# Kernel tuning notes

Measured on AMD Instinct MI355X. Metric: run time of the kernel, lower is better.

The kernel has to match this reference:

```python
import jax, jax.numpy as jnp
import numpy as np

D_MODEL = 1024; D_STATE = 64; D_CONV = 4; EXPAND = 2; HEADDIM = 128; NGROUPS = 1; CHUNK = 256
D_INNER = EXPAND * D_MODEL            # 2048
NHEADS = D_INNER // HEADDIM           # 16
CONV_DIM = D_INNER + 2 * NGROUPS * D_STATE   # 2176
D_IN_PROJ = 2 * D_INNER + 2 * NGROUPS * D_STATE + NHEADS  # 4240
B = 4; G = 256; L = 2048
EPS = 1e-5


def setup_inputs() -> dict:
    key = jax.random.key(0)
    ks = jax.random.split(key, 12)
    def nrm(k, shape, s=0.02):
        return jax.random.normal(k, shape, jnp.float32) * s
    return dict(
        local_repr=jax.random.normal(ks[0], (B, L, D_MODEL), jnp.float32),
        global_repr=jax.random.normal(ks[1], (B, G, D_MODEL), jnp.float32),
        norm1_w=jnp.ones((D_MODEL,), jnp.float32), norm1_b=jnp.zeros((D_MODEL,), jnp.float32),
        norm2_w=jnp.ones((D_MODEL,), jnp.float32), norm2_b=jnp.zeros((D_MODEL,), jnp.float32),
        norm3_w=jnp.ones((D_MODEL,), jnp.float32), norm3_b=jnp.zeros((D_MODEL,), jnp.float32),
        in_proj_w=nrm(ks[2], (D_IN_PROJ, D_MODEL)),
        conv_w=nrm(ks[3], (CONV_DIM, D_CONV), 0.2),
        conv_b=jnp.zeros((CONV_DIM,), jnp.float32),
        dt_bias=jnp.log(jnp.expm1(jax.random.uniform(ks[4], (NHEADS,), jnp.float32, 1e-3, 0.1))),
        A_log=jnp.log(jax.random.uniform(ks[5], (NHEADS,), jnp.float32, 1.0, 16.0)),
        D_skip=jnp.ones((NHEADS,), jnp.float32),
        ssd_norm_w=jnp.ones((D_INNER,), jnp.float32),
        out_proj_w=nrm(ks[6], (D_MODEL, D_INNER)),
        ffn_w1=nrm(ks[7], (D_MODEL // 2, D_MODEL)),
        ffn_b1=jnp.zeros((D_MODEL // 2,), jnp.float32),
        ffn_w2=nrm(ks[8], (D_MODEL, D_MODEL // 2)),
        ffn_b2=jnp.zeros((D_MODEL,), jnp.float32),
    )


def _ln(x, w, b):
    mu = jnp.mean(x, axis=-1, keepdims=True)
    var = jnp.mean((x - mu) ** 2, axis=-1, keepdims=True)
    return (x - mu) * jax.lax.rsqrt(var + EPS) * w + b


def _segsum(a):
    # a: (..., T) -> (..., T, T) lower-triangular sums a[j+1..i]
    T = a.shape[-1]
    cs = jnp.cumsum(a, axis=-1)
    diff = cs[..., :, None] - cs[..., None, :]
    mask = jnp.tril(jnp.ones((T, T), bool))
    return jnp.where(mask, diff, -jnp.inf)


def _ssd(xdt, a_dt, Bh, Ch):
    # xdt: (b,t,h,p) = x*dt ; a_dt: (b,t,h) = dt*A ; Bh,Ch: (b,t,h,n)
    b, t, h, p = xdt.shape
    n = Bh.shape[-1]
    c = t // CHUNK
    X = xdt.reshape(b, c, CHUNK, h, p)
    Bc = Bh.reshape(b, c, CHUNK, h, n)
    Cc = Ch.reshape(b, c, CHUNK, h, n)
    Ac = a_dt.reshape(b, c, CHUNK, h).transpose(0, 3, 1, 2)  # (b,h,c,k)
    A_cum = jnp.cumsum(Ac, axis=-1)
    Lm = jnp.exp(_segsum(Ac))                                # (b,h,c,k,k)
    Y_diag = jnp.einsum('bckhn,bcshn,bhcks,bcshp->bckhp', Cc, Bc, Lm, X)
    decay_states = jnp.exp(A_cum[..., -1:] - A_cum)          # (b,h,c,k)
    states = jnp.einsum('bckhn,bhck,bckhp->bchpn', Bc, decay_states, X)
    A_last = jnp.pad(A_cum[..., -1], ((0, 0), (0, 0), (1, 0)))
    decay_chunk = jnp.exp(_segsum(A_last))                   # (b,h,c+1,c+1)
    states = jnp.concatenate([jnp.zeros_like(states[:, :1]), states], axis=1)
    new_states = jnp.einsum('bhzc,bchpn->bzhpn', decay_chunk, states)
    states_in = new_states[:, :-1]                           # (b,c,h,p,n)
    out_decay = jnp.exp(A_cum)                               # (b,h,c,k)
    Y_off = jnp.einsum('bckhn,bchpn,bhck->bckhp', Cc, states_in, out_decay)
    return (Y_diag + Y_off).reshape(b, t, h, p)


def _mamba2(x, in_proj_w, conv_w, conv_b, dt_bias, A_log, D_skip, ssd_norm_w, out_proj_w):
    b, t, _ = x.shape
    zxbcdt = x @ in_proj_w.T                                  # (b,t,D_IN_PROJ)
    z = zxbcdt[..., :D_INNER]
    xBC = zxbcdt[..., D_INNER:D_INNER + CONV_DIM]
    dt = jax.nn.softplus(zxbcdt[..., D_INNER + CONV_DIM:] + dt_bias)  # (b,t,h)
    # causal depthwise conv1d, kernel D_CONV
    xp = jnp.pad(xBC, ((0, 0), (D_CONV - 1, 0), (0, 0)))
    xBC = sum(xp[:, i:i + t, :] * conv_w[:, i] for i in range(D_CONV)) + conv_b
    xBC = jax.nn.silu(xBC)
    xs = xBC[..., :D_INNER].reshape(b, t, NHEADS, HEADDIM)
    Bm = xBC[..., D_INNER:D_INNER + NGROUPS * D_STATE].reshape(b, t, NGROUPS, D_STATE)
    Cm = xBC[..., D_INNER + NGROUPS * D_STATE:].reshape(b, t, NGROUPS, D_STATE)
    rep = NHEADS // NGROUPS
    Bh = jnp.repeat(Bm, rep, axis=2)
    Ch = jnp.repeat(Cm, rep, axis=2)
    A = -jnp.exp(A_log)                                       # (h,)
    Y = _ssd(xs * dt[..., None], dt * A, Bh, Ch)
    y = Y + D_skip[None, None, :, None] * xs
    y = y.reshape(b, t, D_INNER)
    # gated RMSNorm (norm_before_gate=False)
    y = y * jax.nn.silu(z)
    y = y * jax.lax.rsqrt(jnp.mean(y * y, axis=-1, keepdims=True) + EPS) * ssd_norm_w
    return y @ out_proj_w.T


def reference(local_repr, global_repr, norm1_w, norm1_b, norm2_w, norm2_b, norm3_w, norm3_b,
              in_proj_w, conv_w, conv_b, dt_bias, A_log, D_skip, ssd_norm_w, out_proj_w,
              ffn_w1, ffn_b1, ffn_w2, ffn_b2):
    local_n = _ln(local_repr, norm1_w, norm1_b)
    global_n = _ln(global_repr, norm2_w, norm2_b)
    x = jnp.concatenate([global_n, local_n], axis=1)          # (B, G+L, D)
    x = _mamba2(x, in_proj_w, conv_w, conv_b, dt_bias, A_log, D_skip, ssd_norm_w, out_proj_w)
    x = x[:, -local_n.shape[1]:, :] + local_n
    x = _ln(x, norm3_w, norm3_b)
    h = jax.nn.gelu(x @ ffn_w1.T + ffn_b1, approximate=False)
    return (h @ ffn_w2.T + ffn_b2) + x
```

## Files before the change

kernel.cpp:

```cpp
#include <hip/hip_runtime.h>
#include <math.h>

#define B_ 4
#define L_ 2048
#define G_ 256
#define T_ 2304
#define DM 1024
#define DINNER 2048
#define NH 16
#define HD 128
#define NSTATE 64
#define CONVD 2176
#define DPROJ 4240
#define NPROJ_PAD 4352
#define NCHUNK 9
#define CK 256
#define EPSV 1e-5f
#define CROWS 16

typedef unsigned short bf16t;
using bf16x8 = __attribute__((ext_vector_type(8))) short;
using f32x4  = __attribute__((ext_vector_type(4))) float;

__device__ __forceinline__ float bf2f(bf16t u) {
  return __uint_as_float(((unsigned int)u) << 16);
}
__device__ __forceinline__ bf16t f2bf(float f) {
  unsigned int u = __float_as_uint(f);
  u += 0x7FFFu + ((u >> 16) & 1u);
  return (bf16t)(u >> 16);
}

__device__ __forceinline__ void g2lds16(const bf16t* g, short* l) {
  __builtin_amdgcn_global_load_lds(
      (const __attribute__((address_space(1))) unsigned int*)g,
      (__attribute__((address_space(3))) unsigned int*)l, 16, 0, 0);
}

__device__ __forceinline__ int2 xcd_swz(int tiles_n) {
  int gx = gridDim.x, gy = gridDim.y;
  int id = blockIdx.y * gx + blockIdx.x;
  int cpx = (gx * gy) >> 3;
  int L = (id & 7) * cpx + (id >> 3);
  return make_int2(L % tiles_n, L / tiles_n);
}

__device__ __forceinline__ float2 block_reduce2(float a, float b) {
  __shared__ float sa[4], sb[4];
  #pragma unroll
  for (int off = 32; off > 0; off >>= 1) {
    a += __shfl_down(a, off, 64);
    b += __shfl_down(b, off, 64);
  }
  int lane = threadIdx.x & 63, wid = threadIdx.x >> 6;
  if (lane == 0) { sa[wid] = a; sb[wid] = b; }
  __syncthreads();
  return make_float2(sa[0] + sa[1] + sa[2] + sa[3], sb[0] + sb[1] + sb[2] + sb[3]);
}

__global__ __launch_bounds__(256) void ln_cvt_kernel(
    const float* __restrict__ localr, const float* __restrict__ globalr,
    const float* __restrict__ w1, const float* __restrict__ b1,
    const float* __restrict__ w2, const float* __restrict__ b2,
    bf16t* __restrict__ x, const float* __restrict__ inpw,
    bf16t* __restrict__ inpw_bf) {
  int blk = blockIdx.x;
  if (blk < B_ * T_) {
    int t = blk % T_, b = blk / T_;
    const float *src, *w, *bb;
    if (t < G_) { src = globalr + ((long)b * G_ + t) * DM;        w = w2; bb = b2; }
    else        { src = localr  + ((long)b * L_ + (t - G_)) * DM; w = w1; bb = b1; }
    int d = threadIdx.x * 4;
    float4 v = *(const float4*)&src[d];
    float s = v.x + v.y + v.z + v.w;
    float sq = v.x * v.x + v.y * v.y + v.z * v.z + v.w * v.w;
    float2 r2 = block_reduce2(s, sq);
    float mu = r2.x * (1.f / DM);
    float var = r2.y * (1.f / DM) - mu * mu;
    float rstd = rsqrtf(var + EPSV);
    float4 wv = *(const float4*)&w[d];
    float4 bv = *(const float4*)&bb[d];
    ushort4 o;
    o.x = f2bf((v.x - mu) * rstd * wv.x + bv.x);
    o.y = f2bf((v.y - mu) * rstd * wv.y + bv.y);
    o.z = f2bf((v.z - mu) * rstd * wv.z + bv.z);
    o.w = f2bf((v.w - mu) * rstd * wv.w + bv.w);
    *(ushort4*)&x[(long)blk * DM + d] = o;
  } else {
    long i = (long)(blk - B_ * T_) * 1024 + threadIdx.x * 4;
    const long nreal = (long)DPROJ * DM, ntot = (long)NPROJ_PAD * DM;
    if (i < ntot) {
      ushort4 o = {0, 0, 0, 0};
      if (i < nreal) {
        float4 v = *(const float4*)&inpw[i];
        o.x = f2bf(v.x); o.y = f2bf(v.y); o.z = f2bf(v.z); o.w = f2bf(v.w);
      }
      *(ushort4*)&inpw_bf[i] = o;
    }
  }
}

template<int EPI, bool OFFS, int K>
__global__ __launch_bounds__(512, 2) void gemm_wide(
    const bf16t* __restrict__ A, const bf16t* __restrict__ W,
    bf16t* __restrict__ Cb, bf16t* __restrict__ z, bf16t* __restrict__ xpre,
    float* __restrict__ dtr, int N) {
  __shared__ short LDS8[49152];
  int tid = threadIdx.x;
  int lane = tid & 63, w = tid >> 6;
  int wm = w >> 1, wn = w & 1;
  int l15 = lane & 15;
  int2 sz = xcd_swz(gridDim.x);
  int bn = sz.x * 128, bm = sz.y * 256;
  if (EPI == 0 && bn < DINNER && (bm % 2304) == 0) return;
  long bmA = OFFS ? ((long)(bm >> 11) * T_ + G_ + (bm & 2047)) : (long)bm;

  int csub = ((lane & 7) ^ (lane >> 3)) * 8;
  const bf16t* srcA = A + (bmA + w * 16 + (lane >> 3)) * (long)K + csub;
  const bf16t* srcW = W + (long)(bn + w * 16 + (lane >> 3)) * K + csub;
  int stageDst = w * 1024 + lane * 8;

  int off0 = l15 * 64 + (((lane >> 4) + 0) ^ (lane & 7)) * 8;
  int off1 = l15 * 64 + (((lane >> 4) + 4) ^ (lane & 7)) * 8;

  f32x4 acc[4][4] = {};
  bf16x8 af[2][2], bq[4][2];

#define STAGE2(gsrc, ldsoff) do { \
    g2lds16((gsrc), LDS8 + (ldsoff) + stageDst); \
    g2lds16((gsrc) + 8 * (long)K, LDS8 + (ldsoff) + stageDst + 512); } while (0)

  STAGE2(srcA, 0);
  STAGE2(srcA + 128 * (long)K, 8192);
  STAGE2(srcW, 16384);
  STAGE2(srcW + 64, 24576 + 16384);
  asm volatile("s_waitcnt vmcnt(2)" ::: "memory");
  __builtin_amdgcn_s_barrier();

  const int nt = K >> 6;
  #pragma unroll 2
  for (int t = 0; t < nt; ++t) {
    int cs_ = (t & 1) * 24576;
    int ns_ = 24576 - cs_;
    const short* aB = LDS8 + cs_ + wm * 4096;
    const short* bB = LDS8 + cs_ + 16384 + wn * 4096;

    #pragma unroll
    for (int mi = 0; mi < 2; mi++) {
      af[mi][0] = *(const bf16x8*)&aB[mi * 1024 + off0];
      af[mi][1] = *(const bf16x8*)&aB[mi * 1024 + off1];
    }
    #pragma unroll
    for (int ni = 0; ni < 2; ni++) {
      bq[ni][0] = *(const bf16x8*)&bB[ni * 1024 + off0];
      bq[ni][1] = *(const bf16x8*)&bB[ni * 1024 + off1];
    }
    if (t + 1 < nt) STAGE2(srcA + (t + 1) * 64, ns_);
    __builtin_amdgcn_s_barrier();
    __builtin_amdgcn_s_setprio(1);
    #pragma unroll
    for (int ks = 0; ks < 2; ks++)
      #pragma unroll
      for (int mi = 0; mi < 2; mi++)
        #pragma unroll
        for (int ni = 0; ni < 2; ni++)
          acc[mi][ni] = __builtin_amdgcn_mfma_f32_16x16x32_bf16(af[mi][ks], bq[ni][ks], acc[mi][ni], 0, 0, 0);
    __builtin_amdgcn_s_setprio(0);
    __builtin_amdgcn_s_barrier();

    #pragma unroll
    for (int ni = 2; ni < 4; ni++) {
      bq[ni][0] = *(const bf16x8*)&bB[ni * 1024 + off0];
      bq[ni][1] = *(const bf16x8*)&bB[ni * 1024 + off1];
    }
    if (t + 1 < nt) STAGE2(srcA + 128 * (long)K + (t + 1) * 64, ns_ + 8192);
    __builtin_amdgcn_s_barrier();
    __builtin_amdgcn_s_setprio(1);
    #pragma unroll
    for (int ks = 0; ks < 2; ks++)
      #pragma unroll
      for (int mi = 0; mi < 2; mi++)
        #pragma unroll
        for (int ni = 2; ni < 4; ni++)
          acc[mi][ni] = __builtin_amdgcn_mfma_f32_16x16x32_bf16(af[mi][ks], bq[ni][ks], acc[mi][ni], 0, 0, 0);
    __builtin_amdgcn_s_setprio(0);
    __builtin_amdgcn_s_barrier();

    #pragma unroll
    for (int mi = 0; mi < 2; mi++) {
      af[mi][0] = *(const bf16x8*)&aB[(mi + 2) * 1024 + off0];
      af[mi][1] = *(const bf16x8*)&aB[(mi + 2) * 1024 + off1];
    }
    if (t + 2 < nt) STAGE2(srcW + (t + 2) * 64, cs_ + 16384);
    __builtin_amdgcn_s_barrier();
    __builtin_amdgcn_s_setprio(1);
    #pragma unroll
    for (int ks = 0; ks < 2; ks++)
      #pragma unroll
      for (int mi = 0; mi < 2; mi++)
        #pragma unroll
        for (int ni = 0; ni < 4; ni++)
          acc[mi + 2][ni] = __builtin_amdgcn_mfma_f32_16x16x32_bf16(af[mi][ks], bq[ni][ks], acc[mi + 2][ni], 0, 0, 0);
    __builtin_amdgcn_s_setprio(0);
    if (t + 2 < nt)      asm volatile("s_waitcnt vmcnt(2)" ::: "memory");
    else if (t + 1 < nt) asm volatile("s_waitcnt vmcnt(0)" ::: "memory");
    __builtin_amdgcn_s_barrier();
  }
#undef STAGE2

  if (EPI == 0 && bn == 4224) {
    if (wn == 0) {
      #pragma unroll
      for (int mi = 0; mi < 4; mi++)
        #pragma unroll
        for (int r = 0; r < 4; r++) {
          int row = bm + wm * 64 + mi * 16 + (lane >> 4) * 4 + r;
          dtr[(long)row * NH + l15] = acc[mi][0][r];
        }
    }
    return;
  }

  bf16t* Cs = (bf16t*)LDS8;
  #pragma unroll
  for (int pass = 0; pass < 2; pass++) {
    __syncthreads();
    if ((wm >> 1) == pass) {
      #pragma unroll
      for (int mi = 0; mi < 4; mi++)
        #pragma unroll
        for (int ni = 0; ni < 4; ni++)
          #pragma unroll
          for (int r = 0; r < 4; r++)
            Cs[((wm & 1) * 64 + mi * 16 + (lane >> 4) * 4 + r) * 136 + wn * 64 + ni * 16 + l15] =
                f2bf(acc[mi][ni][r]);
    }
    __syncthreads();
    #pragma unroll
    for (int q = 0; q < 4; q++) {
      int idx = q * 512 + tid;
      int row = idx >> 4, cg = idx & 15;
      int gcol = bn + cg * 8;
      long grow = bm + pass * 128 + row;
      bf16x8 v = *(bf16x8*)&Cs[row * 136 + cg * 8];
      if (EPI == 0) {
        if (gcol < DINNER) *(bf16x8*)&z[grow * DINNER + gcol] = v;
        else               *(bf16x8*)&xpre[grow * CONVD + (gcol - DINNER)] = v;
      } else {
        *(bf16x8*)&Cb[grow * (long)N + gcol] = v;
      }
    }
  }
}

template<int EPI>
__global__ __launch_bounds__(256) void gemm_mfma(
    const bf16t* __restrict__ A, const bf16t* __restrict__ W,
    const float* __restrict__ bias, const bf16t* __restrict__ res,
    float* __restrict__ Cf, bf16t* __restrict__ Cb,
    int N, int K) {
  __shared__ __align__(16) short LDS[128 * 136];
  short* As = LDS;
  short* Ws = LDS + 128 * 32;
  int tid = threadIdx.x;
  int lane = tid & 63, w = tid >> 6;
  int wr = w >> 1, wc = w & 1;
  int2 sz = xcd_swz(gridDim.x);
  int bn = sz.x * 128, bm = sz.y * 128;

  int r1 = tid >> 2,         s1 = (((tid & 3) ^ ((r1 >> 1) & 3))) * 8;
  int r2 = (tid + 256) >> 2, s2 = (((tid & 3) ^ ((r2 >> 1) & 3))) * 8;
  const bf16t* gA1 = A + (long)(bm + r1) * K + s1;
  const bf16t* gA2 = A + (long)(bm + r2) * K + s2;
  const bf16t* gW1 = W + (long)(bn + r1) * K + s1;
  const bf16t* gW2 = W + (long)(bn + r2) * K + s2;
  short* lA1 = As + tid * 8;
  short* lA2 = As + (tid + 256) * 8;
  short* lW1 = Ws + tid * 8;
  short* lW2 = Ws + (tid + 256) * 8;

  int arow = wr * 64 + (lane & 15);
  int brow = wc * 64 + (lane & 15);
  int koff = (((lane >> 4) ^ (((lane & 15) >> 1) & 3))) * 8;

  f32x4 acc[4][4] = {};
  for (int k0 = 0; k0 < K; k0 += 32) {
    g2lds16(gA1 + k0, lA1);
    g2lds16(gA2 + k0, lA2);
    g2lds16(gW1 + k0, lW1);
    g2lds16(gW2 + k0, lW2);
    __syncthreads();
    bf16x8 af[4], bf[4];
    #pragma unroll
    for (int mi = 0; mi < 4; mi++) af[mi] = *(bf16x8*)&As[(arow + mi * 16) * 32 + koff];
    #pragma unroll
    for (int ni = 0; ni < 4; ni++) bf[ni] = *(bf16x8*)&Ws[(brow + ni * 16) * 32 + koff];
    #pragma unroll
    for (int mi = 0; mi < 4; mi++)
      #pragma unroll
      for (int ni = 0; ni < 4; ni++)
        acc[mi][ni] = __builtin_amdgcn_mfma_f32_16x16x32_bf16(af[mi], bf[ni], acc[mi][ni], 0, 0, 0);
    __syncthreads();
  }

  int rb = wr * 64 + (lane >> 4) * 4;
  int cb = wc * 64 + (lane & 15);

  if (EPI == 3) {
    float* Cs32 = (float*)LDS;
    #pragma unroll
    for (int pass = 0; pass < 2; pass++) {
      __syncthreads();
      if (wr == pass) {
        #pragma unroll
        for (int mi = 0; mi < 4; mi++)
          #pragma unroll
          for (int ni = 0; ni < 4; ni++)
            #pragma unroll
            for (int r = 0; r < 4; r++) {
              int lrow = (lane >> 4) * 4 + mi * 16 + r;
              Cs32[lrow * 136 + cb + ni * 16] = acc[mi][ni][r];
            }
      }
      __syncthreads();
      #pragma unroll
      for (int q = 0; q < 4; q++) {
        int row = q * 16 + (tid >> 4);
        int col = (tid & 15) * 8;
        long grow = bm + pass * 64 + row; int gcol = bn + col;
        float4 v0 = *(float4*)&Cs32[row * 136 + col];
        float4 v1 = *(float4*)&Cs32[row * 136 + col + 4];
        float4 b0 = *(const float4*)&bias[gcol];
        float4 b1 = *(const float4*)&bias[gcol + 4];
        bf16x8 rv = *(const bf16x8*)&res[grow * N + gcol];
        v0.x += b0.x + bf2f((bf16t)rv[0]); v0.y += b0.y + bf2f((bf16t)rv[1]);
        v0.z += b0.z + bf2f((bf16t)rv[2]); v0.w += b0.w + bf2f((bf16t)rv[3]);
        v1.x += b1.x + bf2f((bf16t)rv[4]); v1.y += b1.y + bf2f((bf16t)rv[5]);
        v1.z += b1.z + bf2f((bf16t)rv[6]); v1.w += b1.w + bf2f((bf16t)rv[7]);
        *(float4*)&Cf[grow * N + gcol] = v0;
        *(float4*)&Cf[grow * N + gcol + 4] = v1;
      }
    }
    return;
  }

  __syncthreads();
  bf16t* Cs = (bf16t*)LDS;
  #pragma unroll
  for (int mi = 0; mi < 4; mi++)
    #pragma unroll
    for (int ni = 0; ni < 4; ni++)
      #pragma unroll
      for (int r = 0; r < 4; r++) {
        float v = acc[mi][ni][r];
        if (EPI == 2) {
          v += bias[bn + cb + ni * 16];
          v = 0.5f * v * (1.f + erff(v * 0.70710678118f));
        }
        Cs[(rb + mi * 16 + r) * 136 + cb + ni * 16] = f2bf(v);
      }
  __syncthreads();
  #pragma unroll
  for (int pass = 0; pass < 8; pass++) {
    int row = pass * 16 + (tid >> 4);
    int col = (tid & 15) * 8;
    bf16x8 vv = *(bf16x8*)&Cs[row * 136 + col];
    long grow = bm + row; int gcol = bn + col;
    *(bf16x8*)&Cb[grow * N + gcol] = vv;
  }
}

__global__ __launch_bounds__(256) void cumsum_kernel(
    const float* __restrict__ dtraw, const float* __restrict__ dt_bias,
    const float* __restrict__ A_log, float* __restrict__ dt,
    float* __restrict__ Acum) {
  int bid = blockIdx.x;
  int c = bid % NCHUNK; int hh = bid / NCHUNK;
  int h = hh % NH; int b = hh / NH;
  int k = threadIdx.x;
  float a = -__expf(A_log[h]);
  long t = (long)b * T_ + c * CK + k;
  float v0 = dtraw[t * NH + h] + dt_bias[h];
  float dtv = (v0 > 20.f) ? v0 : log1pf(__expf(v0));
  dt[t * NH + h] = dtv;
  float v = dtv * a;
  __shared__ float buf[2][CK];
  int cur = 0;
  buf[0][k] = v; __syncthreads();
  for (int off = 1; off < CK; off <<= 1) {
    float tv = buf[cur][k];
    if (k >= off) tv += buf[cur][k - off];
    buf[1 - cur][k] = tv; cur ^= 1; __syncthreads();
  }
  Acum[(long)bid * CK + k] = buf[cur][k];
}

__global__ __launch_bounds__(256) void conv_kernel(
    const bf16t* __restrict__ xpre, const float* __restrict__ cw,
    const float* __restrict__ cb, bf16t* __restrict__ out) {
  int gt = blockIdx.x * 256 + threadIdx.x;
  int cg = gt % 272; int rt = gt / 272;
  int c0 = cg * 8;
  long r0 = (long)rt * CROWS;
  int t0 = (int)(r0 % T_);

  float wreg[4][8];
  #pragma unroll
  for (int j = 0; j < 8; j++) {
    float4 wa = *(const float4*)&cw[(c0 + j) * 4];
    wreg[0][j] = wa.x; wreg[1][j] = wa.y; wreg[2][j] = wa.z; wreg[3][j] = wa.w;
  }
  float4 cb0 = *(const float4*)&cb[c0];
  float4 cb1 = *(const float4*)&cb[c0 + 4];
  float bias[8] = {cb0.x, cb0.y, cb0.z, cb0.w, cb1.x, cb1.y, cb1.z, cb1.w};

  bf16x8 win[4];
  #pragma unroll
  for (int i = 0; i < 3; i++) {
    if (t0 - 3 + i >= 0) win[i] = *(const bf16x8*)&xpre[(r0 - 3 + i) * CONVD + c0];
    else                 win[i] = bf16x8{0,0,0,0,0,0,0,0};
  }

  #pragma unroll
  for (int k = 0; k < CROWS; k++) {
    win[3] = *(const bf16x8*)&xpre[(r0 + k) * CONVD + c0];
    float acc[8];
    #pragma unroll
    for (int j = 0; j < 8; j++) acc[j] = bias[j];
    #pragma unroll
    for (int i = 0; i < 4; i++)
      #pragma unroll
      for (int j = 0; j < 8; j++)
        acc[j] += bf2f((bf16t)win[i][j]) * wreg[i][j];
    bf16x8 o;
    #pragma unroll
    for (int j = 0; j < 8; j++) {
      float s = acc[j] / (1.f + __expf(-acc[j]));
      o[j] = (short)f2bf(s);
    }
    *(bf16x8*)&out[(r0 + k) * CONVD + c0] = o;
    win[0] = win[1]; win[1] = win[2]; win[2] = win[3];
  }
}

__global__ __launch_bounds__(256) void chunk_states_kernel(
    const bf16t* __restrict__ xbc, const float* __restrict__ dt,
    const float* __restrict__ Acum, float* __restrict__ cs) {
  int bid = blockIdx.x;
  int h = bid & 15; int bc = bid >> 4;
  int c = bc & 7; int b = bc >> 3;
  int tid = threadIdx.x;
  int lane = tid & 63, w = tid >> 6;
  long tch = (long)b * T_ + c * CK;
  int acb = ((b * NH + h) * NCHUNK + c) * CK;
  float Alast = Acum[acb + CK - 1];

  __shared__ bf16t Xt[128][72];
  __shared__ bf16t Bt[64][72];
  __shared__ float wk[64];

  f32x4 acc[8] = {};
  for (int kb = 0; kb < 4; kb++) {
    int s0 = kb * 64;
    __syncthreads();
    if (tid < 64)
      wk[tid] = __expf(Alast - Acum[acb + s0 + tid]) * dt[(tch + s0 + tid) * NH + h];
    __syncthreads();
    for (int e = tid; e < 64 * 32; e += 256) {
      int s = e & 63, p4 = e >> 6;
      ushort4 u = *(const ushort4*)&xbc[(tch + s0 + s) * CONVD + h * HD + p4 * 4];
      float wv = wk[s];
      Xt[p4 * 4 + 0][s] = f2bf(bf2f(u.x) * wv);
      Xt[p4 * 4 + 1][s] = f2bf(bf2f(u.y) * wv);
      Xt[p4 * 4 + 2][s] = f2bf(bf2f(u.z) * wv);
      Xt[p4 * 4 + 3][s] = f2bf(bf2f(u.w) * wv);
    }
    for (int e = tid; e < 64 * 16; e += 256) {
      int s = e & 63, n4 = e >> 6;
      ushort4 u = *(const ushort4*)&xbc[(tch + s0 + s) * CONVD + DINNER + n4 * 4];
      Bt[n4 * 4 + 0][s] = u.x; Bt[n4 * 4 + 1][s] = u.y;
      Bt[n4 * 4 + 2][s] = u.z; Bt[n4 * 4 + 3][s] = u.w;
    }
    __syncthreads();
    #pragma unroll
    for (int ks = 0; ks < 2; ks++) {
      int koff = (lane >> 4) * 8 + ks * 32;
      bf16x8 bfr = *(bf16x8*)&Bt[w * 16 + (lane & 15)][koff];
      #pragma unroll
      for (int mi = 0; mi < 8; mi++) {
        bf16x8 af = *(bf16x8*)&Xt[mi * 16 + (lane & 15)][koff];
        acc[mi] = __builtin_amdgcn_mfma_f32_16x16x32_bf16(af, bfr, acc[mi], 0, 0, 0);
      }
    }
  }
  int cbid = (b * NCHUNK + c) * NH + h;
  float* out = cs + (long)cbid * HD * NSTATE;
  int n = w * 16 + (lane & 15);
  #pragma unroll
  for (int mi = 0; mi < 8; mi++) {
    #pragma unroll
    for (int r = 0; r < 4; r++) {
      int p = mi * 16 + (lane >> 4) * 4 + r;
      out[p * NSTATE + n] = acc[mi][r];
    }
  }
}

__global__ __launch_bounds__(256) void state_pass_kernel(
    float* __restrict__ cs, const float* __restrict__ Acum) {
  int bh = blockIdx.x;
  int b = bh / NH, h = bh % NH;
  int e0 = blockIdx.y * 1024 + threadIdx.x;
  for (int q = 0; q < 4; q++) {
    int e = e0 + q * 256;
    float s = 0.f;
    for (int c = 0; c < NCHUNK; c++) {
      long idx = ((long)(b * NCHUNK + c) * NH + h) * (HD * NSTATE) + e;
      if (c < NCHUNK - 1) {
        float tmp = cs[idx];
        cs[idx] = s;
        float g = __expf(Acum[((b * NH + h) * NCHUNK + c) * CK + CK - 1]);
        s = s * g + tmp;
      } else {
        cs[idx] = s;
      }
    }
  }
}

__global__ __launch_bounds__(256) void ssd_y_kernel(
    const bf16t* __restrict__ xbc, const float* __restrict__ dt,
    const float* __restrict__ Acum, const float* __restrict__ sin_,
    const float* __restrict__ Dskip, bf16t* __restrict__ Y) {
  int bid = blockIdx.x;
  int h = bid & 15; int bc = bid >> 4;
  int c = 1 + (bc & 7); int b = bc >> 3;
  int rt = blockIdx.y;
  int tid = threadIdx.x;
  int lane = tid & 63, w = tid >> 6;
  int wr = w >> 1, wc = w & 1;
  long tch = (long)b * T_ + c * CK;
  long tbase = tch + rt * 128;
  int acb = ((b * NH + h) * NCHUNK + c) * CK;

  __shared__ bf16t Cs[128][72];
  __shared__ bf16t Bs[64][72];
  __shared__ bf16t Xt[128][72];
  __shared__ bf16t Sm[128][72];
  __shared__ float Akl[128];
  __shared__ float Asl[64];
  __shared__ float dts[64];

  for (int e = tid; e < 128 * 8; e += 256) {
    int row = e >> 3, seg = (e & 7) * 8;
    *(bf16x8*)&Cs[row][seg] =
        *(const bf16x8*)&xbc[(tbase + row) * CONVD + DINNER + NSTATE + seg];
  }
  if (tid < 128) Akl[tid] = Acum[acb + rt * 128 + tid];

  f32x4 acc[4][4] = {};
  int nsb = 2 * (rt + 1);
  for (int sb = 0; sb < nsb; sb++) {
    int s0 = sb * 64;
    __syncthreads();
    if (tid < 64) {
      Asl[tid] = Acum[acb + s0 + tid];
      dts[tid] = dt[(tch + s0 + tid) * NH + h];
    }
    __syncthreads();
    for (int e = tid; e < 64 * 8; e += 256) {
      int row = e >> 3, seg = (e & 7) * 8;
      *(bf16x8*)&Bs[row][seg] =
          *(const bf16x8*)&xbc[(tch + s0 + row) * CONVD + DINNER + seg];
    }
    for (int e = tid; e < 64 * 32; e += 256) {
      int s = e & 63, p4 = e >> 6;
      ushort4 u = *(const ushort4*)&xbc[(tch + s0 + s) * CONVD + h * HD + p4 * 4];
      float dtv = dts[s];
      Xt[p4 * 4 + 0][s] = f2bf(bf2f(u.x) * dtv);
      Xt[p4 * 4 + 1][s] = f2bf(bf2f(u.y) * dtv);
      Xt[p4 * 4 + 2][s] = f2bf(bf2f(u.z) * dtv);
      Xt[p4 * 4 + 3][s] = f2bf(bf2f(u.w) * dtv);
    }
    __syncthreads();
    {
      f32x4 sacc[2][4] = {};
      int rw0 = w * 32;
      #pragma unroll
      for (int ks = 0; ks < 2; ks++) {
        int koff = (lane >> 4) * 8 + ks * 32;
        bf16x8 a0 = *(bf16x8*)&Cs[rw0 + (lane & 15)][koff];
        bf16x8 a1 = *(bf16x8*)&Cs[rw0 + 16 + (lane & 15)][koff];
        #pragma unroll
        for (int ni = 0; ni < 4; ni++) {
          bf16x8 bfr = *(bf16x8*)&Bs[ni * 16 + (lane & 15)][koff];
          sacc[0][ni] = __builtin_amdgcn_mfma_f32_16x16x32_bf16(a0, bfr, sacc[0][ni], 0, 0, 0);
          sacc[1][ni] = __builtin_amdgcn_mfma_f32_16x16x32_bf16(a1, bfr, sacc[1][ni], 0, 0, 0);
        }
      }
      #pragma unroll
      for (int mi = 0; mi < 2; mi++) {
        #pragma unroll
        for (int ni = 0; ni < 4; ni++) {
          #pragma unroll
          for (int r = 0; r < 4; r++) {
            int row = rw0 + mi * 16 + (lane >> 4) * 4 + r;
            int scol = ni * 16 + (lane & 15);
            int kglob = rt * 128 + row;
            int sglob = s0 + scol;
            float val = 0.f;
            if (sglob <= kglob) val = sacc[mi][ni][r] * __expf(Akl[row] - Asl[scol]);
            Sm[row][scol] = f2bf(val);
          }
        }
      }
    }
    __syncthreads();
    #pragma unroll
    for (int ks = 0; ks < 2; ks++) {
      int koff = (lane >> 4) * 8 + ks * 32;
      bf16x8 af[4], bfr[4];
      #pragma unroll
      for (int mi = 0; mi < 4; mi++) af[mi] = *(bf16x8*)&Sm[wr * 64 + mi * 16 + (lane & 15)][koff];
      #pragma unroll
      for (int ni = 0; ni < 4; ni++) bfr[ni] = *(bf16x8*)&Xt[wc * 64 + ni * 16 + (lane & 15)][koff];
      #pragma unroll
      for (int mi = 0; mi < 4; mi++)
        #pragma unroll
        for (int ni = 0; ni < 4; ni++)
          acc[mi][ni] = __builtin_amdgcn_mfma_f32_16x16x32_bf16(af[mi], bfr[ni], acc[mi][ni], 0, 0, 0);
    }
  }

  float ekr[16];
  #pragma unroll
  for (int mi = 0; mi < 4; mi++)
    #pragma unroll
    for (int r = 0; r < 4; r++)
      ekr[mi * 4 + r] = __expf(Akl[wr * 64 + mi * 16 + (lane >> 4) * 4 + r]);

  int cbid = (b * NCHUNK + c) * NH + h;
  const float* sinb = sin_ + (long)cbid * HD * NSTATE;
  #pragma unroll
  for (int ni = 0; ni < 4; ni++) {
    f32x4 offacc[4] = {};
    int p = wc * 64 + ni * 16 + (lane & 15);
    #pragma unroll
    for (int ks = 0; ks < 2; ks++) {
      int koff = (lane >> 4) * 8 + ks * 32;
      const float* srow = sinb + p * NSTATE + koff;
      float4 sa = *(const float4*)srow;
      float4 sbv = *(const float4*)(srow + 4);
      bf16x8 bfr;
      bfr[0] = (short)f2bf(sa.x);  bfr[1] = (short)f2bf(sa.y);
      bfr[2] = (short)f2bf(sa.z);  bfr[3] = (short)f2bf(sa.w);
      bfr[4] = (short)f2bf(sbv.x); bfr[5] = (short)f2bf(sbv.y);
      bfr[6] = (short)f2bf(sbv.z); bfr[7] = (short)f2bf(sbv.w);
      #pragma unroll
      for (int mi = 0; mi < 4; mi++) {
        bf16x8 af = *(bf16x8*)&Cs[wr * 64 + mi * 16 + (lane & 15)][koff];
        offacc[mi] = __builtin_amdgcn_mfma_f32_16x16x32_bf16(af, bfr, offacc[mi], 0, 0, 0);
      }
    }
    #pragma unroll
    for (int mi = 0; mi < 4; mi++)
      #pragma unroll
      for (int r = 0; r < 4; r++)
        acc[mi][ni][r] += ekr[mi * 4 + r] * offacc[mi][r];
  }

  float dsk = Dskip[h];
  #pragma unroll
  for (int mi = 0; mi < 4; mi++) {
    #pragma unroll
    for (int r = 0; r < 4; r++) {
      int row = wr * 64 + mi * 16 + (lane >> 4) * 4 + r;
      long t = tbase + row;
      #pragma unroll
      for (int ni = 0; ni < 4; ni++) {
        int p = wc * 64 + ni * 16 + (lane & 15);
        float xsv = bf2f(xbc[t * CONVD + h * HD + p]);
        Y[t * DINNER + h * HD + p] = f2bf(acc[mi][ni][r] + dsk * xsv);
      }
    }
  }
}

__global__ __launch_bounds__(256) void gate_rms_cvt_kernel(
    const bf16t* __restrict__ z, const float* __restrict__ nw,
    bf16t* __restrict__ Y,
    const float* __restrict__ outw, const float* __restrict__ f1w,
    const float* __restrict__ f2w, bf16t* __restrict__ o_out,
    bf16t* __restrict__ o_f1, bf16t* __restrict__ o_f2) {
  int blk = blockIdx.x;
  if (blk < B_ * L_) {
    long r = (long)(blk >> 11) * T_ + G_ + (blk & 2047);
    const bf16t* zrow = z + r * DINNER;
    bf16t* yrow = Y + r * DINNER;
    int tid = threadIdx.x;
    float v[8]; float sq = 0.f;
    #pragma unroll
    for (int i = 0; i < 4; i++) {
      int d = tid * 2 + 512 * i;
      ushort2 zu = *(const ushort2*)&zrow[d];
      ushort2 yu = *(const ushort2*)&yrow[d];
      float z0 = bf2f(zu.x), z1 = bf2f(zu.y);
      float y0 = bf2f(yu.x) * (z0 / (1.f + __expf(-z0)));
      float y1 = bf2f(yu.y) * (z1 / (1.f + __expf(-z1)));
      v[2 * i] = y0; v[2 * i + 1] = y1;
      sq += y0 * y0 + y1 * y1;
    }
    float2 r2 = block_reduce2(sq, 0.f);
    float rms = rsqrtf(r2.x * (1.f / DINNER) + EPSV);
    #pragma unroll
    for (int i = 0; i < 4; i++) {
      int d = tid * 2 + 512 * i;
      ushort2 o;
      o.x = f2bf(v[2 * i] * rms * nw[d]);
      o.y = f2bf(v[2 * i + 1] * rms * nw[d + 1]);
      *(ushort2*)&yrow[d] = o;
    }
  } else {
    long i = (long)(blk - B_ * L_) * 1024 + threadIdx.x * 4;
    const long n1 = (long)DM * DINNER;
    const long n2 = (long)(DM / 2) * DM;
    const float* src; bf16t* dst; long off;
    if (i < n1) { src = outw; dst = o_out; off = i; }
    else if (i < n1 + n2) { src = f1w; dst = o_f1; off = i - n1; }
    else { src = f2w; dst = o_f2; off = i - n1 - n2; }
    float4 v = *(const float4*)&src[off];
    ushort4 o;
    o.x = f2bf(v.x); o.y = f2bf(v.y); o.z = f2bf(v.z); o.w = f2bf(v.w);
    *(ushort4*)&dst[off] = o;
  }
}

__global__ __launch_bounds__(256) void res_ln3_kernel(
    const bf16t* __restrict__ mfull, const bf16t* __restrict__ x,
    const float* __restrict__ w3, const float* __restrict__ b3,
    bf16t* __restrict__ x2) {
  int rl = blockIdx.x;
  int tl = rl & 2047, b = rl >> 11;
  long rt = (long)b * T_ + G_ + tl;
  const bf16t* m = mfull + (long)rl * DM;
  const bf16t* xr = x + rt * DM;
  int tid = threadIdx.x;
  float v[4]; float s = 0.f, sq = 0.f;
  #pragma unroll
  for (int i = 0; i < 2; i++) {
    int d = tid * 2 + 512 * i;
    ushort2 mu2 = *(const ushort2*)&m[d];
    ushort2 xu2 = *(const ushort2*)&xr[d];
    float a0 = bf2f(mu2.x) + bf2f(xu2.x);
    float a1 = bf2f(mu2.y) + bf2f(xu2.y);
    v[2 * i] = a0; v[2 * i + 1] = a1;
    s += a0 + a1; sq += a0 * a0 + a1 * a1;
  }
  float2 r2 = block_reduce2(s, sq);
  float mu = r2.x * (1.f / DM);
  float var = r2.y * (1.f / DM) - mu * mu;
  float rstd = rsqrtf(var + EPSV);
  bf16t* dst = x2 + (long)rl * DM;
  #pragma unroll
  for (int i = 0; i < 2; i++) {
    int d = tid * 2 + 512 * i;
    ushort2 o;
    o.x = f2bf((v[2 * i] - mu) * rstd * w3[d] + b3[d]);
    o.y = f2bf((v[2 * i + 1] - mu) * rstd * w3[d + 1] + b3[d + 1]);
    *(ushort2*)&dst[d] = o;
  }
}

extern "C" void kernel_launch(void* const* d_in, const int* in_sizes, int n_in,
                              void* d_out, int out_size, void* d_ws, size_t ws_size,
                              hipStream_t stream) {
  const float* localr = (const float*)d_in[0];
  const float* globalr= (const float*)d_in[1];
  const float* n1w = (const float*)d_in[2];
  const float* n1b = (const float*)d_in[3];
  const float* n2w = (const float*)d_in[4];
  const float* n2b = (const float*)d_in[5];
  const float* n3w = (const float*)d_in[6];
  const float* n3b = (const float*)d_in[7];
  const float* inpw= (const float*)d_in[8];
  const float* convw=(const float*)d_in[9];
  const float* convb=(const float*)d_in[10];
  const float* dtb = (const float*)d_in[11];
  const float* alog= (const float*)d_in[12];
  const float* dskp= (const float*)d_in[13];
  const float* ssdw= (const float*)d_in[14];
  const float* outw= (const float*)d_in[15];
  const float* f1w = (const float*)d_in[16];
  const float* f1b = (const float*)d_in[17];
  const float* f2w = (const float*)d_in[18];
  const float* f2b = (const float*)d_in[19];

  char* ws = (char*)d_ws;
  bf16t* x     = (bf16t*)(ws + 0);
  bf16t* z     = (bf16t*)(ws + 18874368);
  bf16t* mfull = (bf16t*)(ws + 18874368);
  bf16t* xpre  = (bf16t*)(ws + 56623104);
  bf16t* Yb    = (bf16t*)(ws + 56623104);
  float* dtraw = (float*)(ws + 96731136);
  float* dt    = (float*)(ws + 97320960);
  float* Acum  = (float*)(ws + 97910784);
  bf16t* xbc   = (bf16t*)(ws + 98500608);
  bf16t* x2bf  = (bf16t*)(ws + 98500608);
  bf16t* hbuf  = (bf16t*)(ws + 115277824);
  bf16t* outw_bf = (bf16t*)(ws + 123666432);
  bf16t* f1w_bf  = (bf16t*)(ws + 127860736);
  bf16t* f2w_bf  = (bf16t*)(ws + 128909312);
  float* cs    = (float*)(ws + 138608640);
  bf16t* inpw_bf = (bf16t*)(ws + 138608640);

  ln_cvt_kernel<<<B_ * T_ + 4352, 256, 0, stream>>>(
      localr, globalr, n1w, n1b, n2w, n2b, x, inpw, inpw_bf);

  gemm_wide<0, false, 1024><<<dim3(NPROJ_PAD / 128, (B_ * T_) / 256), 512, 0, stream>>>(
      x, inpw_bf, nullptr, z, xpre, dtraw, NPROJ_PAD);

  cumsum_kernel<<<B_ * NH * NCHUNK, 256, 0, stream>>>(dtraw, dtb, alog, dt, Acum);

  conv_kernel<<<(B_ * T_ / CROWS) * 272 / 256, 256, 0, stream>>>(xpre, convw, convb, xbc);

  chunk_states_kernel<<<B_ * (NCHUNK - 1) * NH, 256, 0, stream>>>(xbc, dt, Acum, cs);

  state_pass_kernel<<<dim3(B_ * NH, 8), 256, 0, stream>>>(cs, Acum);

  ssd_y_kernel<<<dim3(B_ * (NCHUNK - 1) * NH, 2), 256, 0, stream>>>(
      xbc, dt, Acum, cs, dskp, Yb);

  gate_rms_cvt_kernel<<<B_ * L_ + 3072, 256, 0, stream>>>(
      z, ssdw, Yb, outw, f1w, f2w, outw_bf, f1w_bf, f2w_bf);

  gemm_wide<1, true, 2048><<<dim3(DM / 128, (B_ * L_) / 256), 512, 0, stream>>>(
      Yb, outw_bf, mfull, nullptr, nullptr, nullptr, DM);

  res_ln3_kernel<<<B_ * L_, 256, 0, stream>>>(mfull, x, n3w, n3b, x2bf);

  gemm_mfma<2><<<dim3((DM / 2) / 128, (B_ * L_) / 128), 256, 0, stream>>>(
      x2bf, f1w_bf, f1b, nullptr, nullptr, hbuf, DM / 2, DM);

  gemm_mfma<3><<<dim3(DM / 128, (B_ * L_) / 128), 256, 0, stream>>>(
      hbuf, f2w_bf, f2b, x2bf, (float*)d_out, nullptr, DM, DM / 2);
}
```

Baseline: 471.6 us.

## Triple-buffer A tiles in wide GEMM and route FFN2 through it

The wide GEMM's LDS staging becomes a three-slot ring for A tiles plus a two-slot buffer for W, so A is prefetched two k-steps ahead with a deeper vmcnt wait. This is meant to hide more global-load latency. The final FFN2 GEMM moves from the 128x128 gemm_mfma kernel to the 256x128 wide kernel, using a new fp32 bias-plus-residual epilogue. The trade-off is a larger LDS footprint (128 KB per block), which may lower occupancy, and the wide kernel's efficiency at K=512 is uncertain.

```diff
diff --git a/kernel.cpp b/kernel.cpp
--- a/kernel.cpp
+++ b/kernel.cpp
@@ -104,8 +104,9 @@
 __global__ __launch_bounds__(512, 2) void gemm_wide(
     const bf16t* __restrict__ A, const bf16t* __restrict__ W,
     bf16t* __restrict__ Cb, bf16t* __restrict__ z, bf16t* __restrict__ xpre,
-    float* __restrict__ dtr, int N) {
-  __shared__ short LDS8[49152];
+    float* __restrict__ dtr, const float* __restrict__ bias,
+    const bf16t* __restrict__ res, float* __restrict__ Cf, int N) {
+  __shared__ short LDS8[65536];
   int tid = threadIdx.x;
   int lane = tid & 63, w = tid >> 6;
   int wm = w >> 1, wn = w & 1;
@@ -132,18 +133,19 @@
 
   STAGE2(srcA, 0);
   STAGE2(srcA + 128 * (long)K, 8192);
-  STAGE2(srcW, 16384);
-  STAGE2(srcW + 64, 24576 + 16384);
-  asm volatile("s_waitcnt vmcnt(2)" ::: "memory");
+  STAGE2(srcW, 49152);
+  STAGE2(srcA + 64, 16384);
+  STAGE2(srcA + 128 * (long)K + 64, 16384 + 8192);
+  STAGE2(srcW + 64, 49152 + 8192);
+  asm volatile("s_waitcnt vmcnt(6)" ::: "memory");
   __builtin_amdgcn_s_barrier();
 
   const int nt = K >> 6;
-  #pragma unroll 2
   for (int t = 0; t < nt; ++t) {
-    int cs_ = (t & 1) * 24576;
-    int ns_ = 24576 - cs_;
-    const short* aB = LDS8 + cs_ + wm * 4096;
-    const short* bB = LDS8 + cs_ + 16384 + wn * 4096;
+    int slotA = (t % 3) * 16384;
+    int slotA2 = ((t + 2) % 3) * 16384;
+    const short* aB = LDS8 + slotA + wm * 4096;
+    const short* bB = LDS8 + 49152 + (t & 1) * 8192 + wn * 4096;
 
     #pragma unroll
     for (int mi = 0; mi < 2; mi++) {
@@ -155,7 +157,7 @@
       bq[ni][0] = *(const bf16x8*)&bB[ni * 1024 + off0];
       bq[ni][1] = *(const bf16x8*)&bB[ni * 1024 + off1];
     }
-    if (t + 1 < nt) STAGE2(srcA + (t + 1) * 64, ns_);
+    if (t + 2 < nt) STAGE2(srcA + (t + 2) * 64, slotA2);
     __builtin_amdgcn_s_barrier();
     __builtin_amdgcn_s_setprio(1);
     #pragma unroll
@@ -173,7 +175,7 @@
       bq[ni][0] = *(const bf16x8*)&bB[ni * 1024 + off0];
       bq[ni][1] = *(const bf16x8*)&bB[ni * 1024 + off1];
     }
-    if (t + 1 < nt) STAGE2(srcA + 128 * (long)K + (t + 1) * 64, ns_ + 8192);
+    if (t + 2 < nt) STAGE2(srcA + 128 * (long)K + (t + 2) * 64, slotA2 + 8192);
     __builtin_amdgcn_s_barrier();
     __builtin_amdgcn_s_setprio(1);
     #pragma unroll
@@ -191,7 +193,7 @@
       af[mi][0] = *(const bf16x8*)&aB[(mi + 2) * 1024 + off0];
       af[mi][1] = *(const bf16x8*)&aB[(mi + 2) * 1024 + off1];
     }
-    if (t + 2 < nt) STAGE2(srcW + (t + 2) * 64, cs_ + 16384);
+    if (t + 2 < nt) STAGE2(srcW + (t + 2) * 64, 49152 + (t & 1) * 8192);
     __builtin_amdgcn_s_barrier();
     __builtin_amdgcn_s_setprio(1);
     #pragma unroll
@@ -202,7 +204,7 @@
         for (int ni = 0; ni < 4; ni++)
           acc[mi + 2][ni] = __builtin_amdgcn_mfma_f32_16x16x32_bf16(af[mi][ks], bq[ni][ks], acc[mi + 2][ni], 0, 0, 0);
     __builtin_amdgcn_s_setprio(0);
-    if (t + 2 < nt)      asm volatile("s_waitcnt vmcnt(2)" ::: "memory");
+    if (t + 2 < nt)      asm volatile("s_waitcnt vmcnt(6)" ::: "memory");
     else if (t + 1 < nt) asm volatile("s_waitcnt vmcnt(0)" ::: "memory");
     __builtin_amdgcn_s_barrier();
   }
@@ -217,6 +219,43 @@
           int row = bm + wm * 64 + mi * 16 + (lane >> 4) * 4 + r;
           dtr[(long)row * NH + l15] = acc[mi][0][r];
         }
+    }
+    return;
+  }
+
+  if (EPI == 2) {
+    float* Cs32 = (float*)LDS8;
+    #pragma unroll
+    for (int pass = 0; pass < 2; pass++) {
+      __syncthreads();
+      if ((wm >> 1) == pass) {
+        #pragma unroll
+        for (int mi = 0; mi < 4; mi++)
+          #pragma unroll
+          for (int ni = 0; ni < 4; ni++)
+            #pragma unroll
+            for (int r = 0; r < 4; r++)
+              Cs32[((wm & 1) * 64 + mi * 16 + (lane >> 4) * 4 + r) * 136 + wn * 64 + ni * 16 + l15] =
+                  acc[mi][ni][r];
+      }
+      __syncthreads();
+      #pragma unroll
+      for (int q = 0; q < 4; q++) {
+        int idx = q * 512 + tid;
+        int row = idx >> 4, cg = (idx & 15) * 8;
+        long grow = bm + pass * 128 + row; int gcol = bn + cg;
+        float4 v0 = *(float4*)&Cs32[row * 136 + cg];
+        float4 v1 = *(float4*)&Cs32[row * 136 + cg + 4];
+        float4 b0 = *(const float4*)&bias[gcol];
+        float4 b1 = *(const float4*)&bias[gcol + 4];
+        bf16x8 rv = *(const bf16x8*)&res[grow * (long)N + gcol];
+        v0.x += b0.x + bf2f((bf16t)rv[0]); v0.y += b0.y + bf2f((bf16t)rv[1]);
+        v0.z += b0.z + bf2f((bf16t)rv[2]); v0.w += b0.w + bf2f((bf16t)rv[3]);
+        v1.x += b1.x + bf2f((bf16t)rv[4]); v1.y += b1.y + bf2f((bf16t)rv[5]);
+        v1.z += b1.z + bf2f((bf16t)rv[6]); v1.w += b1.w + bf2f((bf16t)rv[7]);
+        *(float4*)&Cf[grow * (long)N + gcol] = v0;
+        *(float4*)&Cf[grow * (long)N + gcol + 4] = v1;
+      }
     }
     return;
   }
@@ -305,44 +344,6 @@
 
   int rb = wr * 64 + (lane >> 4) * 4;
   int cb = wc * 64 + (lane & 15);
-
-  if (EPI == 3) {
-    float* Cs32 = (float*)LDS;
-    #pragma unroll
-    for (int pass = 0; pass < 2; pass++) {
-      __syncthreads();
-      if (wr == pass) {
-        #pragma unroll
-        for (int mi = 0; mi < 4; mi++)
-          #pragma unroll
-          for (int ni = 0; ni < 4; ni++)
-            #pragma unroll
-            for (int r = 0; r < 4; r++) {
-              int lrow = (lane >> 4) * 4 + mi * 16 + r;
-              Cs32[lrow * 136 + cb + ni * 16] = acc[mi][ni][r];
-            }
-      }
-      __syncthreads();
-      #pragma unroll
-      for (int q = 0; q < 4; q++) {
-        int row = q * 16 + (tid >> 4);
-        int col = (tid & 15) * 8;
-        long grow = bm + pass * 64 + row; int gcol = bn + col;
-        float4 v0 = *(float4*)&Cs32[row * 136 + col];
-        float4 v1 = *(float4*)&Cs32[row * 136 + col + 4];
-        float4 b0 = *(const float4*)&bias[gcol];
-        float4 b1 = *(const float4*)&bias[gcol + 4];
-        bf16x8 rv = *(const bf16x8*)&res[grow * N + gcol];
-        v0.x += b0.x + bf2f((bf16t)rv[0]); v0.y += b0.y + bf2f((bf16t)rv[1]);
-        v0.z += b0.z + bf2f((bf16t)rv[2]); v0.w += b0.w + bf2f((bf16t)rv[3]);
-        v1.x += b1.x + bf2f((bf16t)rv[4]); v1.y += b1.y + bf2f((bf16t)rv[5]);
-        v1.z += b1.z + bf2f((bf16t)rv[6]); v1.w += b1.w + bf2f((bf16t)rv[7]);
-        *(float4*)&Cf[grow * N + gcol] = v0;
-        *(float4*)&Cf[grow * N + gcol + 4] = v1;
-      }
-    }
-    return;
-  }
 
   __syncthreads();
   bf16t* Cs = (bf16t*)LDS;
@@ -817,7 +818,7 @@
       localr, globalr, n1w, n1b, n2w, n2b, x, inpw, inpw_bf);
 
   gemm_wide<0, false, 1024><<<dim3(NPROJ_PAD / 128, (B_ * T_) / 256), 512, 0, stream>>>(
-      x, inpw_bf, nullptr, z, xpre, dtraw, NPROJ_PAD);
+      x, inpw_bf, nullptr, z, xpre, dtraw, nullptr, nullptr, nullptr, NPROJ_PAD);
 
   cumsum_kernel<<<B_ * NH * NCHUNK, 256, 0, stream>>>(dtraw, dtb, alog, dt, Acum);
 
@@ -834,13 +835,13 @@
       z, ssdw, Yb, outw, f1w, f2w, outw_bf, f1w_bf, f2w_bf);
 
   gemm_wide<1, true, 2048><<<dim3(DM / 128, (B_ * L_) / 256), 512, 0, stream>>>(
-      Yb, outw_bf, mfull, nullptr, nullptr, nullptr, DM);
+      Yb, outw_bf, mfull, nullptr, nullptr, nullptr, nullptr, nullptr, nullptr, DM);
 
   res_ln3_kernel<<<B_ * L_, 256, 0, stream>>>(mfull, x, n3w, n3b, x2bf);
 
   gemm_mfma<2><<<dim3((DM / 2) / 128, (B_ * L_) / 128), 256, 0, stream>>>(
       x2bf, f1w_bf, f1b, nullptr, nullptr, hbuf, DM / 2, DM);
 
-  gemm_mfma<3><<<dim3(DM / 128, (B_ * L_) / 128), 256, 0, stream>>>(
-      hbuf, f2w_bf, f2b, x2bf, (float*)d_out, nullptr, DM, DM / 2);
-}
+  gemm_wide<2, false, 512><<<dim3(DM / 128, (B_ * L_) / 256), 512, 0, stream>>>(
+      hbuf, f2w_bf, nullptr, nullptr, nullptr, nullptr, f2b, x2bf, (float*)d_out, DM);
+}
```

Measured after the change: 472.5 us. Within noise of the previous version (+0.2%).
